# Kernel tuning notes

Measured on AMD Instinct MI355X. Metric: run time of the kernel, lower is better.

## Reference

```python
import jax, jax.numpy as jnp
import numpy as np

DIM = 1024
NUM_HEADS = 16
HEAD_DIM = DIM // NUM_HEADS
SCALE = 1.0 / float(np.sqrt(HEAD_DIM))


def setup_inputs() -> dict:
    key = jax.random.key(0)
    ks = jax.random.split(key, 8)
    b, n = 1, 4096
    x = jax.random.normal(ks[0], (b, n, DIM), dtype=jnp.float32)
    cos = jax.random.uniform(ks[1], (b, n, HEAD_DIM // 2), dtype=jnp.float32)
    sin = jax.random.uniform(ks[2], (b, n, HEAD_DIM // 2), dtype=jnp.float32)
    # qkv Linear(dim, 3*dim) and proj Linear(dim, dim); store weights as [in, out]
    w_qkv = jax.random.normal(ks[3], (DIM, 3 * DIM), dtype=jnp.float32) * (1.0 / np.sqrt(DIM))
    b_qkv = jax.random.normal(ks[4], (3 * DIM,), dtype=jnp.float32) * 0.01
    w_proj = jax.random.normal(ks[5], (DIM, DIM), dtype=jnp.float32) * (1.0 / np.sqrt(DIM))
    b_proj = jax.random.normal(ks[6], (DIM,), dtype=jnp.float32) * 0.01
    return {"x": x, "cos": cos, "sin": sin, "w_qkv": w_qkv, "b_qkv": b_qkv,
            "w_proj": w_proj, "b_proj": b_proj}


def _rotate_half(t):
    t1, t2 = jnp.split(t, 2, axis=-1)
    return jnp.concatenate([-t2, t1], axis=-1)


def reference(x, cos, sin, w_qkv, b_qkv, w_proj, b_proj):
    b, n, d = x.shape
    qkv = x @ w_qkv + b_qkv                      # [b, n, 3d]
    q, k, v = jnp.split(qkv, 3, axis=-1)
    # [b, n, h, hd] layout (avoids explicit transposes; einsum handles head axis)
    q = q.reshape(b, n, NUM_HEADS, HEAD_DIM)
    k = k.reshape(b, n, NUM_HEADS, HEAD_DIM)
    v = v.reshape(b, n, NUM_HEADS, HEAD_DIM)
    # RoPE: cos/sin [b, n, hd/2] -> [b, n, 1, hd], broadcast over heads
    cos_f = jnp.concatenate([cos, cos], axis=-1)[:, :, None, :]
    sin_f = jnp.concatenate([sin, sin], axis=-1)[:, :, None, :]
    q = q * cos_f + _rotate_half(q) * sin_f
    k = k * cos_f + _rotate_half(k) * sin_f
    # SDPA (non-causal, no dropout in eval)
    scores = jnp.einsum("bqhd,bkhd->bhqk", q, k) * SCALE
    attn = jax.nn.softmax(scores, axis=-1)
    out = jnp.einsum("bhqk,bkhd->bqhd", attn, v).reshape(b, n, d)
    return out @ w_proj + b_proj
```

## Files before the change

### kernel.cpp

```cpp
#include <hip/hip_runtime.h>
#include <hip/hip_bf16.h>
#include <cstdint>


#define TOK 4096
#define DIM_ 1024
#define NHEAD 16
#define HDIM 64
#define N3 3072
#define SCALE_LOG2E 0.18033688011112042f

typedef __bf16 bf16_t;
typedef bf16_t bf16x8 __attribute__((ext_vector_type(8)));
typedef float floatx4 __attribute__((ext_vector_type(4)));

__device__ __forceinline__ void async_ld16(const bf16_t* g, bf16_t* l) {
  __builtin_amdgcn_global_load_lds(
      (const __attribute__((address_space(1))) void*)(g),
      (__attribute__((address_space(3))) void*)(l), 16, 0, 0);
}

__global__ __launch_bounds__(256) void k_cvt(const float* __restrict__ in,
                                             bf16_t* __restrict__ out, int n4) {
  int i = blockIdx.x * 256 + threadIdx.x;
  if (i < n4) {
    float4 v = ((const float4*)in)[i];
    union { bf16_t b[4]; uint64_t u; } p;
    p.b[0] = (bf16_t)v.x; p.b[1] = (bf16_t)v.y;
    p.b[2] = (bf16_t)v.z; p.b[3] = (bf16_t)v.w;
    ((uint64_t*)out)[i] = p.u;
  }
}

__global__ __launch_bounds__(256) void k_tcvt(const float* __restrict__ in,
                                              bf16_t* __restrict__ out, int R, int C) {
  __shared__ float tile[32][33];
  int c0 = blockIdx.x * 32, r0 = blockIdx.y * 32;
  int tx = threadIdx.x & 31, ty = threadIdx.x >> 5;
#pragma unroll
  for (int i = 0; i < 4; i++) {
    int r = ty + i * 8;
    tile[r][tx] = in[(size_t)(r0 + r) * C + c0 + tx];
  }
  __syncthreads();
#pragma unroll
  for (int i = 0; i < 4; i++) {
    int c = ty + i * 8;
    out[(size_t)(c0 + c) * R + r0 + tx] = (bf16_t)tile[tx][c];
  }
}

__global__ __launch_bounds__(256) void k_qkv(
    const bf16_t* __restrict__ A,
    const bf16_t* __restrict__ Bt,
    const float* __restrict__ bias,
    const float* __restrict__ cs,
    const float* __restrict__ sn,
    bf16_t* __restrict__ qb, bf16_t* __restrict__ kb, bf16_t* __restrict__ vT) {
  constexpr int K = 1024, BK = 32;
  __shared__ bf16_t As[128 * BK] __attribute__((aligned(16)));
  __shared__ bf16_t Bs[128 * BK] __attribute__((aligned(16)));
  const int t = threadIdx.x;
  const int lane = t & 63, w = t >> 6;
  const int lrow = lane & 15, quad = lane >> 4;
  const int m0 = blockIdx.y * 128, n0 = blockIdx.x * 128;
  const int wm = (w >> 1) * 64, wn = (w & 1) * 64;

  const floatx4 ZV = {0.f, 0.f, 0.f, 0.f};
  floatx4 acc[4][4];
#pragma unroll
  for (int i = 0; i < 4; i++)
#pragma unroll
    for (int j = 0; j < 4; j++) acc[i][j] = ZV;

  for (int kt = 0; kt < K; kt += BK) {
#pragma unroll
    for (int r = 0; r < 2; r++) {
      int idx = r * 256 + t;
      int lbase = (r * 256 + w * 64) * 8;
      async_ld16(&A[(size_t)(m0 + (idx >> 2)) * K + kt + (idx & 3) * 8], &As[lbase]);
      async_ld16(&Bt[(size_t)(n0 + (idx >> 2)) * K + kt + (idx & 3) * 8], &Bs[lbase]);
    }
    __syncthreads();
    bf16x8 af[4], bf[4];
#pragma unroll
    for (int i = 0; i < 4; i++)
      af[i] = *(const bf16x8*)&As[(wm + i * 16 + lrow) * BK + quad * 8];
#pragma unroll
    for (int i = 0; i < 4; i++)
      bf[i] = *(const bf16x8*)&Bs[(wn + i * 16 + lrow) * BK + quad * 8];
#pragma unroll
    for (int mi = 0; mi < 4; mi++)
#pragma unroll
      for (int ni = 0; ni < 4; ni++)
        acc[mi][ni] = __builtin_amdgcn_mfma_f32_16x16x32_bf16(af[mi], bf[ni], acc[mi][ni], 0, 0, 0);
    __syncthreads();
  }

  const int c0 = n0 + wn;
  const int seg = c0 >> 10;
  const int h = (c0 & 1023) >> 6;
  float bv[4];
#pragma unroll
  for (int ni = 0; ni < 4; ni++) bv[ni] = bias[c0 + ni * 16 + lrow];

  if (seg < 2) {
    bf16_t* base = ((seg == 0) ? qb : kb) + (size_t)h * TOK * HDIM;
    const float qs = (seg == 0) ? SCALE_LOG2E : 1.0f;
#pragma unroll
    for (int mi = 0; mi < 4; mi++) {
#pragma unroll
      for (int reg = 0; reg < 4; reg++) {
        const int r = m0 + wm + mi * 16 + quad * 4 + reg;
        const float c_lo = cs[r * 32 + lrow];
        const float c_hi = cs[r * 32 + 16 + lrow];
        const float s_lo = sn[r * 32 + lrow];
        const float s_hi = sn[r * 32 + 16 + lrow];
        const float v0 = acc[mi][0][reg] + bv[0];
        const float v1 = acc[mi][1][reg] + bv[1];
        const float v2 = acc[mi][2][reg] + bv[2];
        const float v3 = acc[mi][3][reg] + bv[3];
        const float o0 = (v0 * c_lo - v2 * s_lo) * qs;
        const float o1 = (v1 * c_hi - v3 * s_hi) * qs;
        const float o2 = (v2 * c_lo + v0 * s_lo) * qs;
        const float o3 = (v3 * c_hi + v1 * s_hi) * qs;
        bf16_t* rp = base + (size_t)r * HDIM + lrow;
        rp[0]  = (bf16_t)o0;
        rp[16] = (bf16_t)o1;
        rp[32] = (bf16_t)o2;
        rp[48] = (bf16_t)o3;
      }
    }
  } else {
    bf16_t* base = vT + (size_t)h * HDIM * TOK;
#pragma unroll
    for (int mi = 0; mi < 4; mi++) {
      const int rbase = m0 + wm + mi * 16 + quad * 4;
#pragma unroll
      for (int ni = 0; ni < 4; ni++) {
        union { bf16_t b[4]; uint64_t u; } p;
#pragma unroll
        for (int reg = 0; reg < 4; reg++) p.b[reg] = (bf16_t)(acc[mi][ni][reg] + bv[ni]);
        *(uint64_t*)&base[(size_t)(ni * 16 + lrow) * TOK + rbase] = p.u;
      }
    }
  }
}

__global__ __launch_bounds__(128) void k_attn(
    const bf16_t* __restrict__ qb, const bf16_t* __restrict__ kb,
    const bf16_t* __restrict__ vT, bf16_t* __restrict__ ao) {
  __shared__ bf16_t Ks[2][64 * 64] __attribute__((aligned(16)));
  __shared__ bf16_t Vs[2][64 * 64] __attribute__((aligned(16)));
  __shared__ bf16_t Ps[2][32 * 64] __attribute__((aligned(16)));
  const int t = threadIdx.x, lane = t & 63, w = t >> 6;
  const int lrow = lane & 15, quad = lane >> 4;
  const int h = blockIdx.x & 15;
  const int q0 = (blockIdx.x >> 4) * 64 + w * 32;
  const bf16_t* qh = qb + (size_t)h * TOK * HDIM;
  const bf16_t* kh = kb + (size_t)h * TOK * HDIM;
  const bf16_t* vh = vT + (size_t)h * HDIM * TOK;
  bf16_t* Pw = &Ps[w][0];

  const int ksrc = (t >> 3) * HDIM + (((t & 7) ^ ((t >> 3) & 7)) * 8);
  const int vsrc = (t >> 3) * TOK + (((t & 7) ^ ((t >> 3) & 7)) * 8);

  bf16x8 qf[2][2];
#pragma unroll
  for (int ni = 0; ni < 2; ni++)
#pragma unroll
    for (int ks = 0; ks < 2; ks++)
      qf[ni][ks] = *(const bf16x8*)&qh[(size_t)(q0 + ni * 16 + lrow) * HDIM + ks * 32 + quad * 8];

  const floatx4 ZV = {0.f, 0.f, 0.f, 0.f};
  floatx4 o[4][2];
  float lst[2] = {0.f, 0.f};
#pragma unroll
  for (int d = 0; d < 4; d++)
#pragma unroll
    for (int ni = 0; ni < 2; ni++) o[d][ni] = ZV;

#pragma unroll
  for (int r = 0; r < 4; r++) {
    async_ld16(&kh[(size_t)r * 16 * HDIM + ksrc], &Ks[0][r * 1024 + w * 512]);
    async_ld16(&vh[(size_t)r * 16 * TOK + vsrc], &Vs[0][r * 1024 + w * 512]);
  }

  for (int it = 0; it < TOK / 64; ++it) {
    const int b = it & 1;
    __syncthreads();
    if (it + 1 < TOK / 64) {
      const int j1 = (it + 1) * 64;
#pragma unroll
      for (int r = 0; r < 4; r++) {
        async_ld16(&kh[(size_t)(j1 + r * 16) * HDIM + ksrc], &Ks[b ^ 1][r * 1024 + w * 512]);
        async_ld16(&vh[(size_t)(r * 16) * TOK + j1 + vsrc], &Vs[b ^ 1][r * 1024 + w * 512]);
      }
    }

    floatx4 s[4][2];
#pragma unroll
    for (int mi = 0; mi < 4; mi++)
#pragma unroll
      for (int ni = 0; ni < 2; ni++) s[mi][ni] = ZV;
#pragma unroll
    for (int ks = 0; ks < 2; ks++)
#pragma unroll
      for (int mi = 0; mi < 4; mi++) {
        bf16x8 kf = *(const bf16x8*)&Ks[b][(mi * 16 + lrow) * 64 + (((ks * 4 + quad) ^ (lrow & 7)) * 8)];
#pragma unroll
        for (int ni = 0; ni < 2; ni++)
          s[mi][ni] = __builtin_amdgcn_mfma_f32_16x16x32_bf16(kf, qf[ni][ks], s[mi][ni], 0, 0, 0);
      }

#pragma unroll
    for (int mi = 0; mi < 4; mi++)
#pragma unroll
      for (int ni = 0; ni < 2; ni++)
#pragma unroll
        for (int reg = 0; reg < 4; reg++) {
          float p = __builtin_amdgcn_exp2f(s[mi][ni][reg]);
          s[mi][ni][reg] = p;
          lst[ni] += p;
        }

#pragma unroll
    for (int mi = 0; mi < 4; mi++)
#pragma unroll
      for (int ni = 0; ni < 2; ni++) {
        union { bf16_t b4[4]; uint64_t u; } p;
#pragma unroll
        for (int reg = 0; reg < 4; reg++) p.b4[reg] = (bf16_t)s[mi][ni][reg];
        *(uint64_t*)&Pw[(ni * 16 + lrow) * 64 + (((mi * 4 + quad) ^ lrow) * 4)] = p.u;
      }

#pragma unroll
    for (int ks = 0; ks < 2; ks++) {
      bf16x8 pf[2];
#pragma unroll
      for (int ni = 0; ni < 2; ni++) {
        const int row = (ni * 16 + lrow) * 64;
        const int c0 = ks * 8 + quad * 2;
        union { uint64_t u[2]; bf16x8 v; } pp;
        pp.u[0] = *(const uint64_t*)&Pw[row + ((c0 ^ lrow) * 4)];
        pp.u[1] = *(const uint64_t*)&Pw[row + (((c0 + 1) ^ lrow) * 4)];
        pf[ni] = pp.v;
      }
#pragma unroll
      for (int dt = 0; dt < 4; dt++) {
        bf16x8 vf = *(const bf16x8*)&Vs[b][(dt * 16 + lrow) * 64 + (((ks * 4 + quad) ^ (lrow & 7)) * 8)];
#pragma unroll
        for (int ni = 0; ni < 2; ni++)
          o[dt][ni] = __builtin_amdgcn_mfma_f32_16x16x32_bf16(vf, pf[ni], o[dt][ni], 0, 0, 0);
      }
    }
  }

#pragma unroll
  for (int ni = 0; ni < 2; ni++) {
    float l = lst[ni];
    l += __shfl_xor(l, 16, 64);
    l += __shfl_xor(l, 32, 64);
    const float inv = 1.0f / l;
    const int qrow = q0 + ni * 16 + lrow;
#pragma unroll
    for (int d = 0; d < 4; d++) {
      union { bf16_t b4[4]; uint64_t u; } p;
#pragma unroll
      for (int reg = 0; reg < 4; reg++) p.b4[reg] = (bf16_t)(o[d][ni][reg] * inv);
      *(uint64_t*)&ao[(size_t)qrow * DIM_ + h * HDIM + d * 16 + quad * 4] = p.u;
    }
  }
}

__global__ __launch_bounds__(256) void k_proj(
    const bf16_t* __restrict__ A,
    const bf16_t* __restrict__ Bt,
    const float* __restrict__ bias, float* __restrict__ out) {
  constexpr int K = 1024, BK = 32;
  __shared__ bf16_t As[64 * BK] __attribute__((aligned(16)));
  __shared__ bf16_t Bs[128 * BK] __attribute__((aligned(16)));
  const int t = threadIdx.x;
  const int lane = t & 63, w = t >> 6;
  const int lrow = lane & 15, quad = lane >> 4;
  const int m0 = blockIdx.y * 64, n0 = blockIdx.x * 128;
  const int wm = (w >> 1) * 32, wn = (w & 1) * 64;

  const floatx4 ZV = {0.f, 0.f, 0.f, 0.f};
  floatx4 acc[2][4];
#pragma unroll
  for (int i = 0; i < 2; i++)
#pragma unroll
    for (int j = 0; j < 4; j++) acc[i][j] = ZV;

  for (int kt = 0; kt < K; kt += BK) {
    async_ld16(&A[(size_t)(m0 + (t >> 2)) * K + kt + (t & 3) * 8], &As[w * 512]);
#pragma unroll
    for (int r = 0; r < 2; r++) {
      int idx = r * 256 + t;
      async_ld16(&Bt[(size_t)(n0 + (idx >> 2)) * K + kt + (idx & 3) * 8],
                 &Bs[(r * 256 + w * 64) * 8]);
    }
    __syncthreads();
    bf16x8 af[2], bf[4];
#pragma unroll
    for (int i = 0; i < 2; i++)
      af[i] = *(const bf16x8*)&As[(wm + i * 16 + lrow) * BK + quad * 8];
#pragma unroll
    for (int i = 0; i < 4; i++)
      bf[i] = *(const bf16x8*)&Bs[(wn + i * 16 + lrow) * BK + quad * 8];
#pragma unroll
    for (int mi = 0; mi < 2; mi++)
#pragma unroll
      for (int ni = 0; ni < 4; ni++)
        acc[mi][ni] = __builtin_amdgcn_mfma_f32_16x16x32_bf16(af[mi], bf[ni], acc[mi][ni], 0, 0, 0);
    __syncthreads();
  }

  const int c0 = n0 + wn;
#pragma unroll
  for (int ni = 0; ni < 4; ni++) {
    float bv = bias[c0 + ni * 16 + lrow];
#pragma unroll
    for (int mi = 0; mi < 2; mi++)
#pragma unroll
      for (int reg = 0; reg < 4; reg++) {
        int r = m0 + wm + mi * 16 + quad * 4 + reg;
        out[(size_t)r * DIM_ + c0 + ni * 16 + lrow] = acc[mi][ni][reg] + bv;
      }
  }
}

extern "C" void kernel_launch(void* const* d_in, const int* in_sizes, int n_in,
                              void* d_out, int out_size, void* d_ws, size_t ws_size,
                              hipStream_t stream) {
  const float* x      = (const float*)d_in[0];
  const float* cs     = (const float*)d_in[1];
  const float* sn     = (const float*)d_in[2];
  const float* w_qkv  = (const float*)d_in[3];
  const float* b_qkv  = (const float*)d_in[4];
  const float* w_proj = (const float*)d_in[5];
  const float* b_proj = (const float*)d_in[6];
  float* out = (float*)d_out;

  char* ws = (char*)d_ws;
  bf16_t* xb     = (bf16_t*)(ws);
  bf16_t* wqkvT  = (bf16_t*)(ws + 8388608);
  bf16_t* wprojT = (bf16_t*)(ws + 14680064);
  bf16_t* qb     = (bf16_t*)(ws + 16777216);
  bf16_t* kb     = (bf16_t*)(ws + 25165824);
  bf16_t* vT     = (bf16_t*)(ws + 33554432);
  bf16_t* ao     = xb;

  k_cvt<<<dim3(4096), dim3(256), 0, stream>>>(x, xb, 1048576);
  k_tcvt<<<dim3(96, 32), dim3(256), 0, stream>>>(w_qkv, wqkvT, 1024, 3072);
  k_tcvt<<<dim3(32, 32), dim3(256), 0, stream>>>(w_proj, wprojT, 1024, 1024);
  k_qkv<<<dim3(24, 32), dim3(256), 0, stream>>>(xb, wqkvT, b_qkv, cs, sn, qb, kb, vT);
  k_attn<<<dim3(1024), dim3(128), 0, stream>>>(qb, kb, vT, ao);
  k_proj<<<dim3(8, 64), dim3(256), 0, stream>>>(ao, wprojT, b_proj, out);
}
```

Baseline: 247.2 us.

## Split attention key tiles across two wave pairs and fuse prep conversion kernels

The attention kernel now runs 4 waves per block: two query groups times two key halves of each 64-key tile. Each wave computes half the scores and PV products, and the two key-half partial outputs and row sums are merged through shared memory at the end. This doubles the waves per block to raise MFMA utilisation and latency hiding, at the cost of an extra reduction and more sync. The three input conversion and transpose kernels are merged into one launch to cut launch overhead.

```diff
diff --git a/kernel.cpp b/kernel.cpp
--- a/kernel.cpp
+++ b/kernel.cpp
@@ -20,22 +20,29 @@
       (__attribute__((address_space(3))) void*)(l), 16, 0, 0);
 }
 
-__global__ __launch_bounds__(256) void k_cvt(const float* __restrict__ in,
-                                             bf16_t* __restrict__ out, int n4) {
-  int i = blockIdx.x * 256 + threadIdx.x;
-  if (i < n4) {
-    float4 v = ((const float4*)in)[i];
-    union { bf16_t b[4]; uint64_t u; } p;
-    p.b[0] = (bf16_t)v.x; p.b[1] = (bf16_t)v.y;
-    p.b[2] = (bf16_t)v.z; p.b[3] = (bf16_t)v.w;
-    ((uint64_t*)out)[i] = p.u;
-  }
-}
-
-__global__ __launch_bounds__(256) void k_tcvt(const float* __restrict__ in,
-                                              bf16_t* __restrict__ out, int R, int C) {
+__global__ __launch_bounds__(256) void k_prep(
+    const float* __restrict__ x, const float* __restrict__ w_qkv,
+    const float* __restrict__ w_proj, bf16_t* __restrict__ xb,
+    bf16_t* __restrict__ wqkvT, bf16_t* __restrict__ wprojT) {
   __shared__ float tile[32][33];
-  int c0 = blockIdx.x * 32, r0 = blockIdx.y * 32;
+  const int b = blockIdx.x;
+  if (b < 4096) {
+    int i = b * 256 + threadIdx.x;
+    float4 v = ((const float4*)x)[i];
+    union { bf16_t bb[4]; uint64_t u; } p;
+    p.bb[0] = (bf16_t)v.x; p.bb[1] = (bf16_t)v.y;
+    p.bb[2] = (bf16_t)v.z; p.bb[3] = (bf16_t)v.w;
+    ((uint64_t*)xb)[i] = p.u;
+    return;
+  }
+  const float* in; bf16_t* out; int R, C, c0, r0;
+  if (b < 7168) {
+    int bb = b - 4096; in = w_qkv; out = wqkvT; R = 1024; C = 3072;
+    c0 = (bb % 96) * 32; r0 = (bb / 96) * 32;
+  } else {
+    int bb = b - 7168; in = w_proj; out = wprojT; R = 1024; C = 1024;
+    c0 = (bb % 32) * 32; r0 = (bb / 32) * 32;
+  }
   int tx = threadIdx.x & 31, ty = threadIdx.x >> 5;
 #pragma unroll
   for (int i = 0; i < 4; i++) {
@@ -147,20 +154,20 @@
   }
 }
 
-__global__ __launch_bounds__(128) void k_attn(
+__global__ __launch_bounds__(256, 4) void k_attn(
     const bf16_t* __restrict__ qb, const bf16_t* __restrict__ kb,
     const bf16_t* __restrict__ vT, bf16_t* __restrict__ ao) {
   __shared__ bf16_t Ks[2][64 * 64] __attribute__((aligned(16)));
   __shared__ bf16_t Vs[2][64 * 64] __attribute__((aligned(16)));
-  __shared__ bf16_t Ps[2][32 * 64] __attribute__((aligned(16)));
+  __shared__ bf16_t Ps[64 * 64] __attribute__((aligned(16)));
   const int t = threadIdx.x, lane = t & 63, w = t >> 6;
   const int lrow = lane & 15, quad = lane >> 4;
+  const int qg = w & 1, kh = w >> 1;
   const int h = blockIdx.x & 15;
-  const int q0 = (blockIdx.x >> 4) * 64 + w * 32;
+  const int q0 = (blockIdx.x >> 4) * 64;
   const bf16_t* qh = qb + (size_t)h * TOK * HDIM;
-  const bf16_t* kh = kb + (size_t)h * TOK * HDIM;
-  const bf16_t* vh = vT + (size_t)h * HDIM * TOK;
-  bf16_t* Pw = &Ps[w][0];
+  const bf16_t* khp = kb + (size_t)h * TOK * HDIM;
+  const bf16_t* vhp = vT + (size_t)h * HDIM * TOK;
 
   const int ksrc = (t >> 3) * HDIM + (((t & 7) ^ ((t >> 3) & 7)) * 8);
   const int vsrc = (t >> 3) * TOK + (((t & 7) ^ ((t >> 3) & 7)) * 8);
@@ -170,20 +177,20 @@
   for (int ni = 0; ni < 2; ni++)
 #pragma unroll
     for (int ks = 0; ks < 2; ks++)
-      qf[ni][ks] = *(const bf16x8*)&qh[(size_t)(q0 + ni * 16 + lrow) * HDIM + ks * 32 + quad * 8];
+      qf[ni][ks] = *(const bf16x8*)&qh[(size_t)(q0 + qg * 32 + ni * 16 + lrow) * HDIM + ks * 32 + quad * 8];
 
   const floatx4 ZV = {0.f, 0.f, 0.f, 0.f};
   floatx4 o[4][2];
-  float lst[2] = {0.f, 0.f};
+  floatx4 lacc[2] = {ZV, ZV};
 #pragma unroll
   for (int d = 0; d < 4; d++)
 #pragma unroll
     for (int ni = 0; ni < 2; ni++) o[d][ni] = ZV;
 
 #pragma unroll
-  for (int r = 0; r < 4; r++) {
-    async_ld16(&kh[(size_t)r * 16 * HDIM + ksrc], &Ks[0][r * 1024 + w * 512]);
-    async_ld16(&vh[(size_t)r * 16 * TOK + vsrc], &Vs[0][r * 1024 + w * 512]);
+  for (int r = 0; r < 2; r++) {
+    async_ld16(&khp[(size_t)(r * 32) * HDIM + ksrc], &Ks[0][r * 2048 + t * 8]);
+    async_ld16(&vhp[(size_t)(r * 32) * TOK + vsrc], &Vs[0][r * 2048 + t * 8]);
   }
 
   for (int it = 0; it < TOK / 64; ++it) {
@@ -192,83 +199,101 @@
     if (it + 1 < TOK / 64) {
       const int j1 = (it + 1) * 64;
 #pragma unroll
-      for (int r = 0; r < 4; r++) {
-        async_ld16(&kh[(size_t)(j1 + r * 16) * HDIM + ksrc], &Ks[b ^ 1][r * 1024 + w * 512]);
-        async_ld16(&vh[(size_t)(r * 16) * TOK + j1 + vsrc], &Vs[b ^ 1][r * 1024 + w * 512]);
-      }
-    }
-
-    floatx4 s[4][2];
-#pragma unroll
-    for (int mi = 0; mi < 4; mi++)
+      for (int r = 0; r < 2; r++) {
+        async_ld16(&khp[((size_t)j1 + r * 32) * HDIM + ksrc], &Ks[b ^ 1][r * 2048 + t * 8]);
+        async_ld16(&vhp[(size_t)(r * 32) * TOK + j1 + vsrc], &Vs[b ^ 1][r * 2048 + t * 8]);
+      }
+    }
+
+    floatx4 s[2][2];
+#pragma unroll
+    for (int mi = 0; mi < 2; mi++)
 #pragma unroll
       for (int ni = 0; ni < 2; ni++) s[mi][ni] = ZV;
 #pragma unroll
     for (int ks = 0; ks < 2; ks++)
 #pragma unroll
-      for (int mi = 0; mi < 4; mi++) {
-        bf16x8 kf = *(const bf16x8*)&Ks[b][(mi * 16 + lrow) * 64 + (((ks * 4 + quad) ^ (lrow & 7)) * 8)];
+      for (int mi = 0; mi < 2; mi++) {
+        bf16x8 kf = *(const bf16x8*)&Ks[b][(kh * 32 + mi * 16 + lrow) * 64 + (((ks * 4 + quad) ^ (lrow & 7)) * 8)];
 #pragma unroll
         for (int ni = 0; ni < 2; ni++)
           s[mi][ni] = __builtin_amdgcn_mfma_f32_16x16x32_bf16(kf, qf[ni][ks], s[mi][ni], 0, 0, 0);
       }
 
 #pragma unroll
-    for (int mi = 0; mi < 4; mi++)
-#pragma unroll
-      for (int ni = 0; ni < 2; ni++)
-#pragma unroll
-        for (int reg = 0; reg < 4; reg++) {
-          float p = __builtin_amdgcn_exp2f(s[mi][ni][reg]);
-          s[mi][ni][reg] = p;
-          lst[ni] += p;
-        }
-
-#pragma unroll
-    for (int mi = 0; mi < 4; mi++)
+    for (int mi = 0; mi < 2; mi++)
+#pragma unroll
+      for (int ni = 0; ni < 2; ni++) {
+#pragma unroll
+        for (int reg = 0; reg < 4; reg++)
+          s[mi][ni][reg] = __builtin_amdgcn_exp2f(s[mi][ni][reg]);
+        lacc[ni] += s[mi][ni];
+      }
+
+#pragma unroll
+    for (int mi = 0; mi < 2; mi++)
 #pragma unroll
       for (int ni = 0; ni < 2; ni++) {
         union { bf16_t b4[4]; uint64_t u; } p;
 #pragma unroll
         for (int reg = 0; reg < 4; reg++) p.b4[reg] = (bf16_t)s[mi][ni][reg];
-        *(uint64_t*)&Pw[(ni * 16 + lrow) * 64 + (((mi * 4 + quad) ^ lrow) * 4)] = p.u;
-      }
-
-#pragma unroll
-    for (int ks = 0; ks < 2; ks++) {
-      bf16x8 pf[2];
-#pragma unroll
-      for (int ni = 0; ni < 2; ni++) {
-        const int row = (ni * 16 + lrow) * 64;
-        const int c0 = ks * 8 + quad * 2;
-        union { uint64_t u[2]; bf16x8 v; } pp;
-        pp.u[0] = *(const uint64_t*)&Pw[row + ((c0 ^ lrow) * 4)];
-        pp.u[1] = *(const uint64_t*)&Pw[row + (((c0 + 1) ^ lrow) * 4)];
-        pf[ni] = pp.v;
-      }
-#pragma unroll
-      for (int dt = 0; dt < 4; dt++) {
-        bf16x8 vf = *(const bf16x8*)&Vs[b][(dt * 16 + lrow) * 64 + (((ks * 4 + quad) ^ (lrow & 7)) * 8)];
-#pragma unroll
-        for (int ni = 0; ni < 2; ni++)
-          o[dt][ni] = __builtin_amdgcn_mfma_f32_16x16x32_bf16(vf, pf[ni], o[dt][ni], 0, 0, 0);
-      }
-    }
-  }
-
+        *(uint64_t*)&Ps[(qg * 32 + ni * 16 + lrow) * 64 + (((kh * 8 + mi * 4 + quad) ^ lrow) * 4)] = p.u;
+      }
+
+    bf16x8 pf[2];
+#pragma unroll
+    for (int ni = 0; ni < 2; ni++) {
+      const int row = (qg * 32 + ni * 16 + lrow) * 64;
+      const int c0 = kh * 8 + quad * 2;
+      union { uint64_t u[2]; bf16x8 v; } pp;
+      pp.u[0] = *(const uint64_t*)&Ps[row + ((c0 ^ lrow) * 4)];
+      pp.u[1] = *(const uint64_t*)&Ps[row + (((c0 + 1) ^ lrow) * 4)];
+      pf[ni] = pp.v;
+    }
+#pragma unroll
+    for (int dt = 0; dt < 4; dt++) {
+      bf16x8 vf = *(const bf16x8*)&Vs[b][(dt * 16 + lrow) * 64 + (((kh * 4 + quad) ^ (lrow & 7)) * 8)];
+#pragma unroll
+      for (int ni = 0; ni < 2; ni++)
+        o[dt][ni] = __builtin_amdgcn_mfma_f32_16x16x32_bf16(vf, pf[ni], o[dt][ni], 0, 0, 0);
+    }
+  }
+
+  __syncthreads();
+  float* Mrg = (float*)&Ks[0][0];
+  float* Lmrg = (float*)&Vs[0][0];
+  float lq[2];
 #pragma unroll
   for (int ni = 0; ni < 2; ni++) {
-    float l = lst[ni];
+    float l = lacc[ni][0] + lacc[ni][1] + lacc[ni][2] + lacc[ni][3];
     l += __shfl_xor(l, 16, 64);
     l += __shfl_xor(l, 32, 64);
-    const float inv = 1.0f / l;
-    const int qrow = q0 + ni * 16 + lrow;
-#pragma unroll
-    for (int d = 0; d < 4; d++) {
-      union { bf16_t b4[4]; uint64_t u; } p;
-#pragma unroll
-      for (int reg = 0; reg < 4; reg++) p.b4[reg] = (bf16_t)(o[d][ni][reg] * inv);
-      *(uint64_t*)&ao[(size_t)qrow * DIM_ + h * HDIM + d * 16 + quad * 4] = p.u;
+    lq[ni] = l;
+  }
+  if (kh == 1) {
+#pragma unroll
+    for (int ni = 0; ni < 2; ni++) {
+#pragma unroll
+      for (int dt = 0; dt < 4; dt++)
+        *(floatx4*)&Mrg[(size_t)qg * 2048 + (ni * 16 + lrow) * 64 + dt * 16 + quad * 4] = o[dt][ni];
+      if (quad == 0) Lmrg[qg * 32 + ni * 16 + lrow] = lq[ni];
+    }
+  }
+  __syncthreads();
+  if (kh == 0) {
+#pragma unroll
+    for (int ni = 0; ni < 2; ni++) {
+      const float l = lq[ni] + Lmrg[qg * 32 + ni * 16 + lrow];
+      const float inv = 1.0f / l;
+      const int qrow = q0 + qg * 32 + ni * 16 + lrow;
+#pragma unroll
+      for (int dt = 0; dt < 4; dt++) {
+        floatx4 ov = *(const floatx4*)&Mrg[(size_t)qg * 2048 + (ni * 16 + lrow) * 64 + dt * 16 + quad * 4];
+        union { bf16_t b4[4]; uint64_t u; } p;
+#pragma unroll
+        for (int reg = 0; reg < 4; reg++) p.b4[reg] = (bf16_t)((o[dt][ni][reg] + ov[reg]) * inv);
+        *(uint64_t*)&ao[(size_t)qrow * DIM_ + h * HDIM + dt * 16 + quad * 4] = p.u;
+      }
     }
   }
 }
@@ -352,10 +377,8 @@
   bf16_t* vT     = (bf16_t*)(ws + 33554432);
   bf16_t* ao     = xb;
 
-  k_cvt<<<dim3(4096), dim3(256), 0, stream>>>(x, xb, 1048576);
-  k_tcvt<<<dim3(96, 32), dim3(256), 0, stream>>>(w_qkv, wqkvT, 1024, 3072);
-  k_tcvt<<<dim3(32, 32), dim3(256), 0, stream>>>(w_proj, wprojT, 1024, 1024);
+  k_prep<<<dim3(8192), dim3(256), 0, stream>>>(x, w_qkv, w_proj, xb, wqkvT, wprojT);
   k_qkv<<<dim3(24, 32), dim3(256), 0, stream>>>(xb, wqkvT, b_qkv, cs, sn, qb, kb, vT);
-  k_attn<<<dim3(1024), dim3(128), 0, stream>>>(qb, kb, vT, ao);
+  k_attn<<<dim3(1024), dim3(256), 0, stream>>>(qb, kb, vT, ao);
   k_proj<<<dim3(8, 64), dim3(256), 0, stream>>>(ao, wprojT, b_proj, out);
 }
```

New measurement: 246.5 us. Within noise of the previous version (-0.3%).
